# Optimization experiments

Hardware: AMD Instinct MI355X
Metric: run time of the kernel (lower is better)

The kernel has to match this reference:

```python
import jax, jax.numpy as jnp
import numpy as np

DECAY = 0.99
EPS = 1e-05
COMMIT_COST = 0.25


def setup_inputs() -> dict:
    key = jax.random.key(0)
    k1, k2 = jax.random.split(key)
    z = jax.random.normal(k1, (32, 256, 64, 64), dtype=jnp.float32)
    codebook = jax.random.normal(k2, (512, 256), dtype=jnp.float32)
    n_i = jnp.zeros((512,), dtype=jnp.float32)
    e_i = codebook  # register_buffer('e_i', codebook.data.clone())
    return {"z": z, "codebook": codebook, "n_i": n_i, "e_i": e_i}


def reference(z, codebook, n_i, e_i):
    K, D = codebook.shape
    b = z.shape[0]
    flat = z.reshape(-1, D)  # [N, D]

    dist = (
        jnp.sum(flat * flat, axis=1, keepdims=True)
        + jnp.sum(codebook * codebook, axis=1)
        - 2.0 * (flat @ codebook.T)
    )  # [N, K]
    encoding = jnp.argmin(dist, axis=1)  # [N]

    # one-hot matmul gather == direct gather
    code = codebook[encoding].reshape(z.shape)

    # EMA codebook update (training path, no-grad in the original)
    counts = jax.ops.segment_sum(
        jnp.ones((flat.shape[0],), dtype=flat.dtype), encoding, num_segments=K
    )  # idx.sum(0)
    code_update = jax.ops.segment_sum(flat, encoding, num_segments=K)  # idx.T @ flat
    n_new = DECAY * n_i + (1.0 - DECAY) * counts
    n_new = (n_new + EPS) / (b + K * EPS) * b  # Laplace smoothing (uses batch size b)
    e_new = DECAY * e_i + (1.0 - DECAY) * code_update
    codebook_new = e_new / n_new[:, None]

    commitment_loss = COMMIT_COST * jnp.mean(
        (z - jax.lax.stop_gradient(code)) ** 2
    )
    # straight-through estimator
    code_ste = z + jax.lax.stop_gradient(code - z)
    return (code_ste, commitment_loss, encoding, codebook_new, n_new, e_new)
```

## Files before the change

kernel.cpp:

```cpp
#include <hip/hip_runtime.h>
#include <cfloat>

#define NROWS 131072
#define DIM 256
#define KCODES 512
#define DECAYF 0.99f
#define OMDECAYF 0.01f
#define EPSF 1e-5f
#define BATCHF 32.0f

#define CHUNK 128
#define ROWMASK 0x1FFFF

#define BMW 16
#define BMB 64
#define PLANE_STRIDE (KCODES * DIM)
#define PLANE_BYTES (PLANE_STRIDE * 2)
#define PC2 16
#define NPIECE (KCODES / PC2)
#define PIECE_H_BYTES 8192
#define SBUF_HALF 16384

typedef __attribute__((ext_vector_type(8))) _Float16 half8;
typedef __attribute__((ext_vector_type(4))) float f32x4;


__device__ __forceinline__ void gload_lds16(const void* g, void* l) {
  __builtin_amdgcn_global_load_lds(
      (const __attribute__((address_space(1))) unsigned int*)g,
      (__attribute__((address_space(3))) unsigned int*)l, 16, 0, 0);
}

__global__ __launch_bounds__(256) void cnorm_kernel(const float* __restrict__ cb,
                                                    const float* __restrict__ e_i,
                                                    float* __restrict__ cnorm,
                                                    float* __restrict__ en_out,
                                                    unsigned short* __restrict__ planes) {
  int k = blockIdx.x;
  int t = threadIdx.x;
  size_t idx = (size_t)k * DIM + t;
  float v = cb[idx];
  en_out[idx] = DECAYF * e_i[idx];
  _Float16 h = (_Float16)v;
  float r1 = v - (float)h;
  _Float16 m = (_Float16)r1;
  unsigned short hb, mb;
  __builtin_memcpy(&hb, &h, 2);
  __builtin_memcpy(&mb, &m, 2);
  int tile = k >> 4, cl = k & 15;
  int kc = t >> 5, lk = (t >> 3) & 3, j = t & 7;
  size_t faddr = ((size_t)((tile * 8 + kc) * 64 + lk * 16 + cl)) * 8 + j;
  planes[faddr] = hb;
  planes[PLANE_STRIDE + faddr] = mb;
  float s = v * v;
  for (int off = 32; off > 0; off >>= 1) s += __shfl_down(s, off);
  __shared__ float p[4];
  if ((t & 63) == 0) p[t >> 6] = s;
  __syncthreads();
  if (t == 0) cnorm[k] = (p[0] + p[1]) + (p[2] + p[3]);
}

__global__ __launch_bounds__(256, 4) void argmin_kernel(
    const float* __restrict__ z, const unsigned short* __restrict__ planes,
    const float* __restrict__ cnorm, const float* __restrict__ cb,
    int* __restrict__ enc_int, float* __restrict__ enc_out,
    int* __restrict__ counts, float* __restrict__ code_out,
    float* __restrict__ loss_acc) {
  __shared__ __align__(16) unsigned char sbuf[2 * SBUF_HALF];
  __shared__ float cn_s[KCODES];
  __shared__ int hist[KCODES];
  __shared__ int sm_enc[BMB];
  __shared__ float lds_loss;

  const int tid = threadIdx.x;
  const int w = tid >> 6;
  const int l = tid & 63;
  const int lc = l & 15;
  const int lk = l >> 4;

  hist[tid] = 0;
  hist[tid + 256] = 0;
  cn_s[tid] = cnorm[tid];
  cn_s[tid + 256] = cnorm[tid + 256];
  if (tid == 0) lds_loss = 0.f;

  half8 a_h[8], a_m[8];
  float zn = 0.f;
  {
    int row = blockIdx.x * BMB + w * BMW + lc;
    const float* zr = z + (size_t)row * DIM;
#pragma unroll
    for (int ch = 0; ch < 8; ++ch) {
      float4 v0 = *(const float4*)&zr[ch * 32 + lk * 8];
      float4 v1 = *(const float4*)&zr[ch * 32 + lk * 8 + 4];
      float vv[8] = {v0.x, v0.y, v0.z, v0.w, v1.x, v1.y, v1.z, v1.w};
      half8 hh, mm;
#pragma unroll
      for (int j = 0; j < 8; ++j) {
        float f = vv[j];
        zn += f * f;
        _Float16 hb = (_Float16)f;
        float r1 = f - (float)hb;
        hh[j] = hb;
        mm[j] = (_Float16)r1;
      }
      a_h[ch] = hh; a_m[ch] = mm;
    }
  }
  zn += __shfl_xor(zn, 16);
  zn += __shfl_xor(zn, 32);

  float minv[4];
  int mini[4];
#pragma unroll
  for (int q = 0; q < 4; ++q) { minv[q] = FLT_MAX; mini[q] = 0; }

  const unsigned char* gplanes = (const unsigned char*)planes;

#define STAGE(p, b)                                                              \
  {                                                                              \
    const unsigned char* gh = gplanes + (size_t)(p) * PIECE_H_BYTES;             \
    unsigned char* lb = &sbuf[(b) * SBUF_HALF];                                  \
    _Pragma("unroll")                                                            \
    for (int q = 0; q < 4; ++q) {                                                \
      int c = w * 4 + q;                                                         \
      const unsigned char* g = (w < 2)                                           \
          ? gh + c * 1024 + l * 16                                               \
          : gh + PLANE_BYTES + (c - 8) * 1024 + l * 16;                          \
      gload_lds16(g, lb + c * 1024);                                             \
    }                                                                            \
  }

  STAGE(0, 0);
  __syncthreads();

#pragma unroll 1
  for (int p = 0; p < NPIECE; ++p) {
    const int cur = p & 1;
    if (p + 1 < NPIECE) STAGE(p + 1, cur ^ 1);

    const int lbase = cur * SBUF_HALF;
    f32x4 acc_a = {0.f, 0.f, 0.f, 0.f};
    f32x4 acc_b = {0.f, 0.f, 0.f, 0.f};
#pragma unroll
    for (int kc = 0; kc < 8; ++kc) {
      int o = lbase + kc * 1024 + l * 16;
      half8 bh = *(const half8*)&sbuf[o];
      half8 bm = *(const half8*)&sbuf[o + 8192];
      acc_a = __builtin_amdgcn_mfma_f32_16x16x32_f16(a_h[kc], bh, acc_a, 0, 0, 0);
      acc_b = __builtin_amdgcn_mfma_f32_16x16x32_f16(a_m[kc], bh, acc_b, 0, 0, 0);
      acc_a = __builtin_amdgcn_mfma_f32_16x16x32_f16(a_h[kc], bm, acc_a, 0, 0, 0);
    }
    {
      int code = p * PC2 + lc;
      float cn = cn_s[code];
#pragma unroll
      for (int q = 0; q < 4; ++q) {
        float s0 = cn - 2.f * (acc_a[q] + acc_b[q]);
        if (s0 < minv[q]) { minv[q] = s0; mini[q] = code; }
      }
    }
    __syncthreads();
  }
#undef STAGE


  float lsum = 0.f;
#pragma unroll
  for (int q = 0; q < 4; ++q) {
    float v = minv[q];
    int idx = mini[q];
    for (int off = 1; off < 16; off <<= 1) {
      float ov = __shfl_xor(v, off);
      int oi = __shfl_xor(idx, off);
      if (ov < v || (ov == v && oi < idx)) { v = ov; idx = oi; }
    }
    float znq = __shfl(zn, lk * 4 + q);
    if (lc == 0) {
      int rloc = w * BMW + lk * 4 + q;
      int row = blockIdx.x * BMB + rloc;
      enc_int[row] = idx;
      enc_out[row] = (float)idx;
      sm_enc[rloc] = idx;
      atomicAdd(&hist[idx], 1);
      lsum += znq + v;
    }
  }
  {
    float val = (lc == 0) ? lsum : 0.f;
    val += __shfl_xor(val, 16);
    val += __shfl_xor(val, 32);
    if (l == 0) atomicAdd(&lds_loss, val);
  }
  __syncthreads();

  {
    const float4* cb4 = (const float4*)cb;
    float4* out4 = (float4*)code_out;
    int base = blockIdx.x * (BMB * (DIM / 4));
#pragma unroll
    for (int it = 0; it < 16; ++it) {
      int idx = it * 256 + tid;
      int k = sm_enc[idx >> 6];
      out4[base + idx] = cb4[k * (DIM / 4) + (idx & 63)];
    }
  }

  {
    int h0 = hist[tid];
    if (h0) atomicAdd(&counts[tid], h0);
    int h1 = hist[tid + 256];
    if (h1) atomicAdd(&counts[tid + 256], h1);
  }
  if (tid == 0) atomicAdd(loss_acc, lds_loss);
}

__global__ __launch_bounds__(512) void scan_kernel(
    const int* __restrict__ counts, const float* __restrict__ n_i,
    float* __restrict__ n_new_out, int* __restrict__ cursor,
    const float* __restrict__ loss_acc, float* __restrict__ loss_out) {
  __shared__ int sd[KCODES];
  int t = threadIdx.x;
  int c = counts[t];
  float nn = DECAYF * n_i[t] + OMDECAYF * (float)c;
  nn = (nn + EPSF) / (BATCHF + (float)KCODES * EPSF) * BATCHF;
  n_new_out[t] = nn;
  sd[t] = c;
  __syncthreads();
  for (int off = 1; off < KCODES; off <<= 1) {
    int v = (t >= off) ? sd[t - off] : 0;
    __syncthreads();
    sd[t] += v;
    __syncthreads();
  }
  cursor[t] = sd[t] - c;
  if (t == 0) loss_out[0] = 0.25f * loss_acc[0] / 33554432.0f;
}

__global__ __launch_bounds__(256) void scatter_kernel(
    const int* __restrict__ enc, int* __restrict__ cursor,
    int* __restrict__ rowlist) {
  __shared__ int lcnt[KCODES];
  __shared__ int lbase[KCODES];
  int tid = threadIdx.x;
  int row = blockIdx.x * 256 + tid;
  lcnt[tid] = 0;
  lcnt[tid + 256] = 0;
  __syncthreads();
  int k = enc[row];
  int p = atomicAdd(&lcnt[k], 1);
  __syncthreads();
  int c0 = lcnt[tid];
  if (c0) lbase[tid] = atomicAdd(&cursor[tid], c0);
  int c1 = lcnt[tid + 256];
  if (c1) lbase[tid + 256] = atomicAdd(&cursor[tid + 256], c1);
  __syncthreads();
  rowlist[lbase[k] + p] = (k << 17) | row;
}

__global__ __launch_bounds__(256) void chunk_sum_kernel(
    const float* __restrict__ z, const int* __restrict__ rowlist,
    float* __restrict__ en_out) {
  __shared__ int rl[CHUNK];
  int tid = threadIdx.x;
  int d = tid;
  if (tid < CHUNK) rl[tid] = rowlist[blockIdx.x * CHUNK + tid];
  __syncthreads();
  int cur = rl[0] >> 17;
  float s = 0.f;
  for (int i = 0; i < CHUNK; i += 4) {
    int p0 = rl[i + 0], p1 = rl[i + 1], p2 = rl[i + 2], p3 = rl[i + 3];
    float v0 = z[(size_t)(p0 & ROWMASK) * DIM + d];
    float v1 = z[(size_t)(p1 & ROWMASK) * DIM + d];
    float v2 = z[(size_t)(p2 & ROWMASK) * DIM + d];
    float v3 = z[(size_t)(p3 & ROWMASK) * DIM + d];
    int k;
    k = p0 >> 17;
    if (k != cur) { atomicAdd(&en_out[(size_t)cur * DIM + d], OMDECAYF * s); s = 0.f; cur = k; }
    s += v0;
    k = p1 >> 17;
    if (k != cur) { atomicAdd(&en_out[(size_t)cur * DIM + d], OMDECAYF * s); s = 0.f; cur = k; }
    s += v1;
    k = p2 >> 17;
    if (k != cur) { atomicAdd(&en_out[(size_t)cur * DIM + d], OMDECAYF * s); s = 0.f; cur = k; }
    s += v2;
    k = p3 >> 17;
    if (k != cur) { atomicAdd(&en_out[(size_t)cur * DIM + d], OMDECAYF * s); s = 0.f; cur = k; }
    s += v3;
  }
  atomicAdd(&en_out[(size_t)cur * DIM + d], OMDECAYF * s);
}

__global__ __launch_bounds__(256) void finalize_kernel(
    const float* __restrict__ en, const float* __restrict__ n_new,
    float* __restrict__ cbn_out) {
  int k = blockIdx.x;
  int d = threadIdx.x;
  size_t idx = (size_t)k * DIM + d;
  cbn_out[idx] = en[idx] / n_new[k];
}

extern "C" void kernel_launch(void* const* d_in, const int* in_sizes, int n_in,
                              void* d_out, int out_size, void* d_ws, size_t ws_size,
                              hipStream_t stream) {
  const float* z = (const float*)d_in[0];
  const float* cb = (const float*)d_in[1];
  const float* n_i = (const float*)d_in[2];
  const float* e_i = (const float*)d_in[3];

  float* out = (float*)d_out;
  float* out_code = out;
  float* out_loss = out + 33554432;
  float* out_enc = out + 33554433;
  float* out_cbn = out + 33685505;
  float* out_nn = out + 33816577;
  float* out_en = out + 33817089;

  char* ws = (char*)d_ws;
  float* cnorm = (float*)(ws + 0);
  int* counts = (int*)(ws + 2048);
  float* loss_acc = (float*)(ws + 4096);
  int* cursor = (int*)(ws + 6144);
  int* enc_int = (int*)(ws + 12288);
  int* rowlist = (int*)(ws + 536576);

  unsigned short* planes = (unsigned short*)(ws + 536576);

  hipMemsetAsync(ws + 2048, 0, 4096, stream);

  cnorm_kernel<<<KCODES, 256, 0, stream>>>(cb, e_i, cnorm, out_en, planes);
  argmin_kernel<<<NROWS / BMB, 256, 0, stream>>>(z, planes, cnorm, cb, enc_int,
                                                 out_enc, counts, out_code, loss_acc);
  scan_kernel<<<1, KCODES, 0, stream>>>(counts, n_i, out_nn, cursor, loss_acc, out_loss);
  scatter_kernel<<<NROWS / 256, 256, 0, stream>>>(enc_int, cursor, rowlist);
  chunk_sum_kernel<<<NROWS / CHUNK, 256, 0, stream>>>(z, rowlist, out_en);
  finalize_kernel<<<KCODES, 256, 0, stream>>>(out_en, out_nn, out_cbn);
}
```

Measured before the change: 367.2 us.

## Replace histogram/scan/scatter/segment-sum pipeline with per-code gather-sum kernel

Removes the counts histogram, prefix scan, row scatter, chunked atomic segment sum and finalize kernels. A single kernel with one block per code scans the full encoding array, collects matching rows in shared memory, sums their z rows, and writes e_new, n_new, the new codebook and the loss directly. The aim is to drop launches and global atomics. In exchange, every block re-reads the whole encoding array, and per-block work depends on how many rows each code receives.

```diff
diff --git a/kernel.cpp b/kernel.cpp
--- a/kernel.cpp
+++ b/kernel.cpp
@@ -8,9 +8,6 @@
 #define OMDECAYF 0.01f
 #define EPSF 1e-5f
 #define BATCHF 32.0f
-
-#define CHUNK 128
-#define ROWMASK 0x1FFFF
 
 #define BMW 16
 #define BMB 64
@@ -21,6 +18,9 @@
 #define PIECE_H_BYTES 8192
 #define SBUF_HALF 16384
 
+#define SEG 8192
+#define NSEG (NROWS / SEG)
+
 typedef __attribute__((ext_vector_type(8))) _Float16 half8;
 typedef __attribute__((ext_vector_type(4))) float f32x4;
 
@@ -32,15 +32,12 @@
 }
 
 __global__ __launch_bounds__(256) void cnorm_kernel(const float* __restrict__ cb,
-                                                    const float* __restrict__ e_i,
                                                     float* __restrict__ cnorm,
-                                                    float* __restrict__ en_out,
                                                     unsigned short* __restrict__ planes) {
   int k = blockIdx.x;
   int t = threadIdx.x;
   size_t idx = (size_t)k * DIM + t;
   float v = cb[idx];
-  en_out[idx] = DECAYF * e_i[idx];
   _Float16 h = (_Float16)v;
   float r1 = v - (float)h;
   _Float16 m = (_Float16)r1;
@@ -64,11 +61,9 @@
     const float* __restrict__ z, const unsigned short* __restrict__ planes,
     const float* __restrict__ cnorm, const float* __restrict__ cb,
     int* __restrict__ enc_int, float* __restrict__ enc_out,
-    int* __restrict__ counts, float* __restrict__ code_out,
-    float* __restrict__ loss_acc) {
+    float* __restrict__ code_out, float* __restrict__ loss_acc) {
   __shared__ __align__(16) unsigned char sbuf[2 * SBUF_HALF];
   __shared__ float cn_s[KCODES];
-  __shared__ int hist[KCODES];
   __shared__ int sm_enc[BMB];
   __shared__ float lds_loss;
 
@@ -78,8 +73,6 @@
   const int lc = l & 15;
   const int lk = l >> 4;
 
-  hist[tid] = 0;
-  hist[tid + 256] = 0;
   cn_s[tid] = cnorm[tid];
   cn_s[tid + 256] = cnorm[tid + 256];
   if (tid == 0) lds_loss = 0.f;
@@ -164,7 +157,6 @@
   }
 #undef STAGE
 
-
   float lsum = 0.f;
 #pragma unroll
   for (int q = 0; q < 4; ++q) {
@@ -182,7 +174,6 @@
       enc_int[row] = idx;
       enc_out[row] = (float)idx;
       sm_enc[rloc] = idx;
-      atomicAdd(&hist[idx], 1);
       lsum += znq + v;
     }
   }
@@ -206,98 +197,77 @@
     }
   }
 
-  {
-    int h0 = hist[tid];
-    if (h0) atomicAdd(&counts[tid], h0);
-    int h1 = hist[tid + 256];
-    if (h1) atomicAdd(&counts[tid + 256], h1);
-  }
   if (tid == 0) atomicAdd(loss_acc, lds_loss);
 }
 
-__global__ __launch_bounds__(512) void scan_kernel(
-    const int* __restrict__ counts, const float* __restrict__ n_i,
-    float* __restrict__ n_new_out, int* __restrict__ cursor,
-    const float* __restrict__ loss_acc, float* __restrict__ loss_out) {
-  __shared__ int sd[KCODES];
-  int t = threadIdx.x;
-  int c = counts[t];
-  float nn = DECAYF * n_i[t] + OMDECAYF * (float)c;
-  nn = (nn + EPSF) / (BATCHF + (float)KCODES * EPSF) * BATCHF;
-  n_new_out[t] = nn;
-  sd[t] = c;
+__global__ __launch_bounds__(256) void code_sum_kernel(
+    const float* __restrict__ z, const int* __restrict__ enc,
+    const float* __restrict__ e_i, const float* __restrict__ n_i,
+    const float* __restrict__ loss_acc, float* __restrict__ en_out,
+    float* __restrict__ cbn_out, float* __restrict__ nn_out,
+    float* __restrict__ loss_out) {
+  __shared__ int rows[SEG];
+  __shared__ int lcnt;
+  __shared__ float4 part[256];
+
+  const int k = blockIdx.x;
+  const int tid = threadIdx.x;
+  const int dq = tid & 63;
+  const int g = tid >> 6;
+
+  const int4* enc4 = (const int4*)enc;
+  float4 acc = {0.f, 0.f, 0.f, 0.f};
+  int total = 0;
+
+  for (int s = 0; s < NSEG; ++s) {
+    if (tid == 0) lcnt = 0;
+    __syncthreads();
+    int b4 = s * (SEG / 4);
+#pragma unroll
+    for (int i = 0; i < 8; ++i) {
+      int vi = b4 + i * 256 + tid;
+      int4 e4 = enc4[vi];
+      int rbase = vi * 4;
+      if (e4.x == k) rows[atomicAdd(&lcnt, 1)] = rbase + 0;
+      if (e4.y == k) rows[atomicAdd(&lcnt, 1)] = rbase + 1;
+      if (e4.z == k) rows[atomicAdd(&lcnt, 1)] = rbase + 2;
+      if (e4.w == k) rows[atomicAdd(&lcnt, 1)] = rbase + 3;
+    }
+    __syncthreads();
+    int m = lcnt;
+    total += m;
+    for (int r = g; r < m; r += 4) {
+      const float4* zr = (const float4*)(z + (size_t)rows[r] * DIM);
+      float4 v = zr[dq];
+      acc.x += v.x; acc.y += v.y; acc.z += v.z; acc.w += v.w;
+    }
+    __syncthreads();
+  }
+
+  part[tid] = acc;
   __syncthreads();
-  for (int off = 1; off < KCODES; off <<= 1) {
-    int v = (t >= off) ? sd[t - off] : 0;
-    __syncthreads();
-    sd[t] += v;
-    __syncthreads();
-  }
-  cursor[t] = sd[t] - c;
-  if (t == 0) loss_out[0] = 0.25f * loss_acc[0] / 33554432.0f;
-}
-
-__global__ __launch_bounds__(256) void scatter_kernel(
-    const int* __restrict__ enc, int* __restrict__ cursor,
-    int* __restrict__ rowlist) {
-  __shared__ int lcnt[KCODES];
-  __shared__ int lbase[KCODES];
-  int tid = threadIdx.x;
-  int row = blockIdx.x * 256 + tid;
-  lcnt[tid] = 0;
-  lcnt[tid + 256] = 0;
-  __syncthreads();
-  int k = enc[row];
-  int p = atomicAdd(&lcnt[k], 1);
-  __syncthreads();
-  int c0 = lcnt[tid];
-  if (c0) lbase[tid] = atomicAdd(&cursor[tid], c0);
-  int c1 = lcnt[tid + 256];
-  if (c1) lbase[tid + 256] = atomicAdd(&cursor[tid + 256], c1);
-  __syncthreads();
-  rowlist[lbase[k] + p] = (k << 17) | row;
-}
-
-__global__ __launch_bounds__(256) void chunk_sum_kernel(
-    const float* __restrict__ z, const int* __restrict__ rowlist,
-    float* __restrict__ en_out) {
-  __shared__ int rl[CHUNK];
-  int tid = threadIdx.x;
-  int d = tid;
-  if (tid < CHUNK) rl[tid] = rowlist[blockIdx.x * CHUNK + tid];
-  __syncthreads();
-  int cur = rl[0] >> 17;
-  float s = 0.f;
-  for (int i = 0; i < CHUNK; i += 4) {
-    int p0 = rl[i + 0], p1 = rl[i + 1], p2 = rl[i + 2], p3 = rl[i + 3];
-    float v0 = z[(size_t)(p0 & ROWMASK) * DIM + d];
-    float v1 = z[(size_t)(p1 & ROWMASK) * DIM + d];
-    float v2 = z[(size_t)(p2 & ROWMASK) * DIM + d];
-    float v3 = z[(size_t)(p3 & ROWMASK) * DIM + d];
-    int k;
-    k = p0 >> 17;
-    if (k != cur) { atomicAdd(&en_out[(size_t)cur * DIM + d], OMDECAYF * s); s = 0.f; cur = k; }
-    s += v0;
-    k = p1 >> 17;
-    if (k != cur) { atomicAdd(&en_out[(size_t)cur * DIM + d], OMDECAYF * s); s = 0.f; cur = k; }
-    s += v1;
-    k = p2 >> 17;
-    if (k != cur) { atomicAdd(&en_out[(size_t)cur * DIM + d], OMDECAYF * s); s = 0.f; cur = k; }
-    s += v2;
-    k = p3 >> 17;
-    if (k != cur) { atomicAdd(&en_out[(size_t)cur * DIM + d], OMDECAYF * s); s = 0.f; cur = k; }
-    s += v3;
-  }
-  atomicAdd(&en_out[(size_t)cur * DIM + d], OMDECAYF * s);
-}
-
-__global__ __launch_bounds__(256) void finalize_kernel(
-    const float* __restrict__ en, const float* __restrict__ n_new,
-    float* __restrict__ cbn_out) {
-  int k = blockIdx.x;
-  int d = threadIdx.x;
-  size_t idx = (size_t)k * DIM + d;
-  cbn_out[idx] = en[idx] / n_new[k];
+  if (g == 0) {
+    float4 a = part[dq], b = part[dq + 64], c = part[dq + 128], d = part[dq + 192];
+    float sx = (a.x + b.x) + (c.x + d.x);
+    float sy = (a.y + b.y) + (c.y + d.y);
+    float sz = (a.z + b.z) + (c.z + d.z);
+    float sw = (a.w + b.w) + (c.w + d.w);
+    float nn = DECAYF * n_i[k] + OMDECAYF * (float)total;
+    nn = (nn + EPSF) / (BATCHF + (float)KCODES * EPSF) * BATCHF;
+    if (tid == 0) nn_out[k] = nn;
+    size_t idx = (size_t)k * DIM + dq * 4;
+    float4 ei = *(const float4*)&e_i[idx];
+    float4 en;
+    en.x = DECAYF * ei.x + OMDECAYF * sx;
+    en.y = DECAYF * ei.y + OMDECAYF * sy;
+    en.z = DECAYF * ei.z + OMDECAYF * sz;
+    en.w = DECAYF * ei.w + OMDECAYF * sw;
+    *(float4*)&en_out[idx] = en;
+    float inv = 1.f / nn;
+    float4 cbn = {en.x * inv, en.y * inv, en.z * inv, en.w * inv};
+    *(float4*)&cbn_out[idx] = cbn;
+  }
+  if (k == 0 && tid == 0) loss_out[0] = 0.25f * loss_acc[0] / 33554432.0f;
 }
 
 extern "C" void kernel_launch(void* const* d_in, const int* in_sizes, int n_in,
@@ -318,21 +288,15 @@
 
   char* ws = (char*)d_ws;
   float* cnorm = (float*)(ws + 0);
-  int* counts = (int*)(ws + 2048);
   float* loss_acc = (float*)(ws + 4096);
-  int* cursor = (int*)(ws + 6144);
   int* enc_int = (int*)(ws + 12288);
-  int* rowlist = (int*)(ws + 536576);
-
   unsigned short* planes = (unsigned short*)(ws + 536576);
 
-  hipMemsetAsync(ws + 2048, 0, 4096, stream);
-
-  cnorm_kernel<<<KCODES, 256, 0, stream>>>(cb, e_i, cnorm, out_en, planes);
+  hipMemsetAsync(ws + 4096, 0, 64, stream);
+
+  cnorm_kernel<<<KCODES, 256, 0, stream>>>(cb, cnorm, planes);
   argmin_kernel<<<NROWS / BMB, 256, 0, stream>>>(z, planes, cnorm, cb, enc_int,
-                                                 out_enc, counts, out_code, loss_acc);
-  scan_kernel<<<1, KCODES, 0, stream>>>(counts, n_i, out_nn, cursor, loss_acc, out_loss);
-  scatter_kernel<<<NROWS / 256, 256, 0, stream>>>(enc_int, cursor, rowlist);
-  chunk_sum_kernel<<<NROWS / CHUNK, 256, 0, stream>>>(z, rowlist, out_en);
-  finalize_kernel<<<KCODES, 256, 0, stream>>>(out_en, out_nn, out_cbn);
-}
+                                                 out_enc, out_code, loss_acc);
+  code_sum_kernel<<<KCODES, 256, 0, stream>>>(z, enc_int, e_i, n_i, loss_acc,
+                                              out_en, out_cbn, out_nn, out_loss);
+}
```

New measurement: 1.021 ms. 178% more time.
